# Kernel optimization log

Hardware: AMD Instinct MI355X
Metric: run time of the kernel (lower is better)

The kernel has to match this reference:

```python
import jax, jax.numpy as jnp
import numpy as np

N_WIRES = 14
N_LAYERS = 2
BATCH = 128


def _ry(t):
    # t: scalar or (B,) real angle -> (...,2,2) complex64 RY matrix
    c = jnp.cos(t / 2)
    s = jnp.sin(t / 2)
    m = jnp.stack([jnp.stack([c, -s], -1), jnp.stack([s, c], -1)], -2)
    return m.astype(jnp.complex64)


def _rz(t):
    tc = t.astype(jnp.complex64) if hasattr(t, 'astype') else jnp.asarray(t, jnp.complex64)
    em = jnp.exp(-0.5j * tc)
    ep = jnp.exp(0.5j * tc)
    z = jnp.zeros_like(em)
    return jnp.stack([jnp.stack([em, z], -1), jnp.stack([z, ep], -1)], -2)


def _rx(t):
    c = jnp.cos(t / 2).astype(jnp.complex64)
    s = (-1j) * jnp.sin(t / 2).astype(jnp.complex64)
    return jnp.stack([jnp.stack([c, s], -1), jnp.stack([s, c], -1)], -2)


def _apply_1q(state, mat, w, n):
    # state: (B, 2**n), wire 0 = most significant axis (Pennylane convention)
    B = state.shape[0]
    s = state.reshape(B, 2 ** w, 2, -1)
    if mat.ndim == 2:
        s = jnp.einsum('ij,bajc->baic', mat, s)
    else:  # per-batch matrices (data encoding)
        s = jnp.einsum('bij,bajc->baic', mat, s)
    return s.reshape(B, -1)


def _apply_cnot(state, c, t, n):
    B = state.shape[0]
    p, q = (c, t) if c < t else (t, c)
    s = state.reshape(B, 2 ** p, 2, 2 ** (q - p - 1), 2, 2 ** (n - q - 1))
    if c < t:
        # control at axis 2, target at axis 4; flip target where control==1
        s = jnp.stack([s[:, :, 0], jnp.flip(s[:, :, 1], axis=3)], axis=2)
    else:
        # control at axis 4, target at axis 2
        s = jnp.stack([s[:, :, :, :, 0], jnp.flip(s[:, :, :, :, 1], axis=2)], axis=4)
    return s.reshape(B, -1)


def _circuit(x, params):
    B, n = x.shape
    n_layers = params.shape[0]
    state = jnp.zeros((B, 2 ** n), dtype=jnp.complex64).at[:, 0].set(1.0)
    # data encoding: RY(x[:, w]) on each wire (batched gate matrices)
    for w in range(n):
        state = _apply_1q(state, _ry(x[:, w]), w, n)
    for l in range(n_layers):
        for w in range(n):
            state = _apply_1q(state, _ry(params[l, w, 0]), w, n)
            state = _apply_1q(state, _rz(params[l, w, 1]), w, n)
            state = _apply_1q(state, _rx(params[l, w, 2]), w, n)
        for w in range(n - 1):
            state = _apply_cnot(state, w, w + 1, n)
        state = _apply_cnot(state, n - 1, 0, n)
    probs = state.real ** 2 + state.imag ** 2  # (B, 2**n)
    zs = []
    for w in range(n):
        p = probs.reshape(B, 2 ** w, 2, -1)
        zs.append(p[:, :, 0].sum(axis=(1, 2)) - p[:, :, 1].sum(axis=(1, 2)))
    return jnp.stack(zs, axis=1).astype(jnp.float32)  # (B, n) <Z_w>


def setup_inputs() -> dict:
    key = jax.random.key(0)
    kx, kp = jax.random.split(key)
    x = jax.random.normal(kx, (BATCH, N_WIRES), dtype=jnp.float32)
    params = jax.random.normal(kp, (N_LAYERS, N_WIRES, 3), dtype=jnp.float32)
    return {"x": x, "params": params}


def reference(x, params):
    return _circuit(x, params)
```

## Files before the change

### kernel.cpp

```cpp
#include <hip/hip_runtime.h>

#define NW 14
#define NT 1024
#define BATCH 128

typedef float v2f __attribute__((ext_vector_type(2)));

constexpr unsigned cnot_pc(unsigned j, int c, int t) {
  int pc = 13 - c, pt = 13 - t;
  return j ^ (((j >> pc) & 1u) << pt);
}
constexpr unsigned gperm(unsigned j) {
  j = cnot_pc(j, 13, 0);
  for (int w = 12; w >= 0; --w) j = cnot_pc(j, w, w + 1);
  return j;
}
constexpr unsigned topbit(unsigned x) {
  unsigned h = 1;
  while (x >>= 1) h <<= 1;
  return h;
}

struct CT {
  unsigned M[NW], S[NW], R[NW];
  static constexpr void inv(const unsigned col[NW], unsigned out[NW]) {
    unsigned rm[NW] = {}, ri[NW] = {};
    for (int r = 0; r < NW; ++r) { rm[r] = 0; ri[r] = 1u << r; }
    for (int b = 0; b < NW; ++b)
      for (int r = 0; r < NW; ++r) rm[r] |= ((col[b] >> r) & 1u) << b;
    for (int c = 0; c < NW; ++c) {
      int piv = c;
      while (!((rm[piv] >> c) & 1u)) ++piv;
      unsigned tm = rm[c]; rm[c] = rm[piv]; rm[piv] = tm;
      unsigned ti = ri[c]; ri[c] = ri[piv]; ri[piv] = ti;
      for (int r = 0; r < NW; ++r)
        if (r != c && ((rm[r] >> c) & 1u)) { rm[r] ^= rm[c]; ri[r] ^= ri[c]; }
    }
    for (int r = 0; r < NW; ++r) out[r] = ri[r];
  }
  constexpr CT() : M{}, S{}, R{} {
    unsigned c1[NW] = {}, c2[NW] = {};
    for (int b = 0; b < NW; ++b) { c1[b] = gperm(1u << b); c2[b] = gperm(c1[b]); }
    unsigned i1[NW] = {}, i2[NW] = {};
    inv(c1, i1); inv(c2, i2);
    for (int w = 0; w < NW; ++w) { M[w] = c1[13 - w]; S[w] = i1[13 - w]; R[w] = i2[13 - w]; }
  }
};
static constexpr CT qct{};
static_assert(qct.M[0] == 0x3000u && qct.M[12] == 0x3u && qct.M[13] == 0x3001u, "mask check");
static_assert(qct.M[4] == 0x300u, "mask check");

__device__ __forceinline__ v2f vswap(v2f m) {
  v2f r;
  r.x = -m.y;
  r.y = m.x;
  return r;
}
__device__ __forceinline__ v2f cmulv(v2f a, v2f b) {
  v2f r;
  r.x = fmaf(a.x, b.x, -a.y * b.y);
  r.y = fmaf(a.x, b.y, a.y * b.x);
  return r;
}

__device__ __forceinline__ void make_mat(float ay, float az, float ax_, v2f m[4]) {
  float c, s, ct, st, cr, sr;
  __sincosf(0.5f * ay, &s, &c);
  __sincosf(0.5f * az, &st, &ct);
  __sincosf(0.5f * ax_, &sr, &cr);
  v2f em, ep;
  em.x = ct; em.y = -st;
  ep.x = ct; ep.y = st;
  v2f r00 = c * em, r01 = -s * em, r10 = s * ep, r11 = c * ep;
  v2f isr;
  isr.x = 0.f; isr.y = -sr;
  m[0] = cmulv(isr, r10) + cr * r00;
  m[1] = cmulv(isr, r11) + cr * r01;
  m[2] = cmulv(isr, r00) + cr * r10;
  m[3] = cmulv(isr, r01) + cr * r11;
}

template <int CTRL> __device__ __forceinline__ int dppi(int x) {
  return __builtin_amdgcn_update_dpp(0, x, CTRL, 0xF, 0xF, true);
}
template <unsigned LM> __device__ __forceinline__ float lane_xor1(float x) {
  if constexpr (LM == 0u) return x;
  else if constexpr (LM >= 16u) {
    return __shfl_xor(x, (int)LM, 64);
  } else {
    int v = __float_as_int(x);
    if constexpr ((LM & 0xCu) == 0xCu) v = dppi<0x140>(v);
    else if constexpr ((LM & 0xCu) == 0x4u) v = dppi<0x141>(v);
    else if constexpr ((LM & 0xCu) == 0x8u) v = dppi<0x128>(v);
    constexpr unsigned REM = ((LM & 0xCu) == 0xCu)   ? (LM ^ 0xFu)
                             : ((LM & 0xCu) == 0x4u) ? (LM ^ 0x7u)
                             : ((LM & 0xCu) == 0x8u) ? (LM ^ 0x8u)
                                                     : LM;
    if constexpr (REM != 0u) {
      constexpr int QC = (int)((0u ^ REM) | ((1u ^ REM) << 2) | ((2u ^ REM) << 4) |
                               ((3u ^ REM) << 6));
      v = dppi<QC>(v);
    }
    return __int_as_float(v);
  }
}
template <unsigned LM> __device__ __forceinline__ v2f lane_xor2(v2f v) {
  if constexpr (LM == 0u) return v;
  v2f r;
  r.x = lane_xor1<LM>(v.x);
  r.y = lane_xor1<LM>(v.y);
  return r;
}

template <unsigned RM, unsigned LM, unsigned SR>
__device__ __forceinline__ void gate16(v2f (&a)[16], const v2f* gm, const v2f* gs,
                                       bool st_) {
  const v2f e00 = gm[0], e01 = gm[1], e10 = gm[2], e11 = gm[3];
  const v2f s00 = gs[0], s01 = gs[1], s10 = gs[2], s11 = gs[3];
  const v2f f00 = st_ ? e11 : e00, f01 = st_ ? e10 : e01;
  const v2f f10 = st_ ? e01 : e10, f11 = st_ ? e00 : e11;
  const v2f h00 = st_ ? s11 : s00, h01 = st_ ? s10 : s01;
  const v2f h10 = st_ ? s01 : s10, h11 = st_ ? s00 : s11;
  if constexpr (RM == 0u) {
#pragma unroll
    for (int r = 0; r < 16; ++r) {
      const v2f p = lane_xor2<LM>(a[r]);
      const v2f A = a[r];
      if (__builtin_popcount((unsigned)r & SR) & 1)
        a[r] = A.x * f11 + A.y * h11 + p.x * f10 + p.y * h10;
      else
        a[r] = A.x * f00 + A.y * h00 + p.x * f01 + p.y * h01;
    }
  } else {
    constexpr unsigned HB = topbit(RM);
#pragma unroll
    for (int r = 0; r < 16; ++r) {
      if (r & (int)HB) continue;
      const int r2 = r ^ (int)RM;
      const v2f A = a[r], B = a[r2];
      const v2f pA = lane_xor2<LM>(B), pB = lane_xor2<LM>(A);
      a[r] = (__builtin_popcount((unsigned)r & SR) & 1)
                 ? (A.x * f11 + A.y * h11 + pA.x * f10 + pA.y * h10)
                 : (A.x * f00 + A.y * h00 + pA.x * f01 + pA.y * h01);
      a[r2] = (__builtin_popcount((unsigned)r2 & SR) & 1)
                  ? (B.x * f11 + B.y * h11 + pB.x * f10 + pB.y * h10)
                  : (B.x * f00 + B.y * h00 + pB.x * f01 + pB.y * h01);
    }
  }
}

template <int W>
__device__ __forceinline__ void applyP1(v2f (&a)[16], const v2f* gm, const v2f* gs,
                                        unsigned qb) {
  constexpr unsigned M = qct.M[W], S = qct.S[W];
  static_assert((M & ~0x3FFu) == 0u, "P1 gate out of window");
  gate16<(M & 0xFu), ((M >> 4) & 0x3Fu), (S & 0xFu)>(a, gm, gs, (__popc(qb & S) & 1) != 0);
}
template <int W>
__device__ __forceinline__ void applyP2(v2f (&a)[16], const v2f* gm, const v2f* gs,
                                        unsigned qb) {
  constexpr unsigned M = qct.M[W], S = qct.S[W];
  static_assert((M & ~0x3E01u) == 0u, "P2 gate out of window");
  gate16<((M >> 10) & 0xFu), ((M & 1u) | (((M >> 9) & 1u) << 1)), ((S >> 10) & 0xFu)>(
      a, gm, gs, (__popc(qb & S) & 1) != 0);
}

__global__ __launch_bounds__(NT, 4) void qsim(const float* __restrict__ x,
                                              const float* __restrict__ params,
                                              float* __restrict__ out) {
  __shared__ v2f stx[16384];
  __shared__ v2f v0[NW][2];
  __shared__ v2f g1m[NW][4];
  __shared__ v2f g1s[NW][4];
  __shared__ v2f Ahi[128];
  __shared__ v2f BloP[8][17];
  __shared__ float red[16][NW];

  const int bat = blockIdx.x;
  const int t = threadIdx.x;
  const unsigned ln = (unsigned)t & 63u, wv = (unsigned)t >> 6;

  if (t < 2 * NW) {
    const int layer = (t >= NW);
    const int w = t - layer * NW;
    v2f m[4];
    if (!layer) {
      make_mat(params[w * 3 + 0] + x[bat * NW + w], params[w * 3 + 1], params[w * 3 + 2], m);
      v0[w][0] = m[0];
      v0[w][1] = m[2];
    } else {
      make_mat(params[NW * 3 + w * 3 + 0], params[NW * 3 + w * 3 + 1],
               params[NW * 3 + w * 3 + 2], m);
      g1m[w][0] = m[0]; g1m[w][1] = m[1]; g1m[w][2] = m[2]; g1m[w][3] = m[3];
      g1s[w][0] = vswap(m[0]); g1s[w][1] = vswap(m[1]);
      g1s[w][2] = vswap(m[2]); g1s[w][3] = vswap(m[3]);
    }
  }
  __syncthreads();
  if (t < 128) {
    v2f pa; pa.x = 1.f; pa.y = 0.f;
#pragma unroll
    for (int w = 0; w < 7; ++w) pa = cmulv(pa, v0[w][(t >> (6 - w)) & 1]);
    Ahi[t] = pa;
    v2f pb; pb.x = 1.f; pb.y = 0.f;
#pragma unroll
    for (int w = 7; w < 14; ++w) pb = cmulv(pb, v0[w][(t >> (13 - w)) & 1]);
    BloP[t >> 4][t & 15] = pb;
  }
  __syncthreads();

  v2f a[16];
  {
    const v2f ahi = Ahi[(wv << 3) | (ln >> 3)];
    const v2f ahis = vswap(ahi);
#pragma unroll
    for (int r = 0; r < 16; ++r) {
      const v2f b = BloP[ln & 7][r];
      a[r] = b.x * ahi + b.y * ahis;
    }
  }

  const unsigned qb1 = (ln << 4) | (wv << 10);
  applyP1<12>(a, g1m[12], g1s[12], qb1);
  applyP1<11>(a, g1m[11], g1s[11], qb1);
  applyP1<10>(a, g1m[10], g1s[10], qb1);
  applyP1<9>(a, g1m[9], g1s[9], qb1);
  applyP1<8>(a, g1m[8], g1s[8], qb1);
  applyP1<7>(a, g1m[7], g1s[7], qb1);
  applyP1<6>(a, g1m[6], g1s[6], qb1);
  applyP1<5>(a, g1m[5], g1s[5], qb1);
  applyP1<4>(a, g1m[4], g1s[4], qb1);

  {
    const unsigned bw = (wv << 10) | (ln << 4) | (ln & 0xFu);
#pragma unroll
    for (int r = 0; r < 16; ++r) stx[bw ^ (unsigned)r] = a[r];
  }
  __syncthreads();
  const unsigned qb2 = (ln & 1u) | (((ln >> 2) & 0xFu) << 1) | (wv << 5) |
                       (((ln >> 1) & 1u) << 9);
  {
    const unsigned c2 = ((ln >> 5) & 1u) | ((wv & 7u) << 1);
    const unsigned br = qb2 ^ c2;
#pragma unroll
    for (int r = 0; r < 16; ++r) a[r] = stx[br | ((unsigned)r << 10)];
  }

  applyP2<3>(a, g1m[3], g1s[3], qb2);
  applyP2<2>(a, g1m[2], g1s[2], qb2);
  applyP2<1>(a, g1m[1], g1s[1], qb2);
  applyP2<0>(a, g1m[0], g1s[0], qb2);
  applyP2<13>(a, g1m[13], g1s[13], qb2);

  float T[16];
#pragma unroll
  for (int r = 0; r < 16; ++r) T[r] = fmaf(a[r].x, a[r].x, a[r].y * a[r].y);
#pragma unroll
  for (int s = 1; s < 16; s <<= 1) {
#pragma unroll
    for (int r = 0; r < 16; ++r) {
      if (!(r & s)) {
        float u = T[r], v = T[r ^ s];
        T[r] = u + v;
        T[r ^ s] = u - v;
      }
    }
  }

#pragma unroll
  for (int w = 0; w < NW; ++w) {
    constexpr unsigned Rr[NW] = {qct.R[0], qct.R[1], qct.R[2], qct.R[3], qct.R[4],
                                 qct.R[5], qct.R[6], qct.R[7], qct.R[8], qct.R[9],
                                 qct.R[10], qct.R[11], qct.R[12], qct.R[13]};
    const unsigned R = Rr[w];
    float val = T[(R >> 10) & 0xFu];
    val = (__popc(qb2 & R) & 1) ? -val : val;
    val += lane_xor1<1>(val);
    val += lane_xor1<2>(val);
    { float u = lane_xor1<4>(val); val += u; }
    val += lane_xor1<8>(val);
    val += __shfl_xor(val, 16, 64);
    val += __shfl_xor(val, 32, 64);
    if ((t & 63) == 0) red[wv][w] = val;
  }
  __syncthreads();
  if (t < NW) {
    float s = 0.f;
#pragma unroll
    for (int i = 0; i < 16; ++i) s += red[i][t];
    out[bat * NW + t] = s;
  }
}

extern "C" void kernel_launch(void* const* d_in, const int* in_sizes, int n_in,
                              void* d_out, int out_size, void* d_ws, size_t ws_size,
                              hipStream_t stream) {
  (void)in_sizes; (void)n_in; (void)d_ws; (void)ws_size; (void)out_size;
  const float* x = (const float*)d_in[0];
  const float* params = (const float*)d_in[1];
  float* out = (float*)d_out;
  qsim<<<dim3(BATCH), dim3(NT), 0, stream>>>(x, params, out);
}
```

Baseline: 69.90 us.

## Remap state storage into permuted basis so gates become plain register/DPP pairs

Changes the per-thread index mapping so that each layer-1 gate acts on a single register bit or a single lane bit in a transformed basis, instead of on multi-bit XOR masks with parity-dependent coefficient swaps. Gates split into pure in-register butterflies and DPP lane-exchange gates, and the gate matrices are packed as float4 for wider LDS loads. The initial product-state construction, the LDS transpose addressing and the measurement masks are rewritten for the new basis, with constexpr checks to guard correctness. This aims to cut cross-lane shuffles and per-element selects, at the cost of more complex indexing that is only validated by compile-time asserts.

```diff
diff --git a/kernel.cpp b/kernel.cpp
--- a/kernel.cpp
+++ b/kernel.cpp
@@ -15,10 +15,10 @@
   for (int w = 12; w >= 0; --w) j = cnot_pc(j, w, w + 1);
   return j;
 }
-constexpr unsigned topbit(unsigned x) {
-  unsigned h = 1;
-  while (x >>= 1) h <<= 1;
-  return h;
+constexpr int pcnt(unsigned x) {
+  int c = 0;
+  while (x) { c += (int)(x & 1u); x >>= 1; }
+  return c;
 }
 
 struct CT {
@@ -48,7 +48,52 @@
 };
 static constexpr CT qct{};
 static_assert(qct.M[0] == 0x3000u && qct.M[12] == 0x3u && qct.M[13] == 0x3001u, "mask check");
-static_assert(qct.M[4] == 0x300u, "mask check");
+
+constexpr unsigned p1f(unsigned b) {
+  return ((b ^ (b >> 1)) ^ ((b & 1u) * 0x3000u)) & 0x3FFFu;
+}
+constexpr bool chk_p1_formula() {
+  for (unsigned b = 0; b < 16384u; ++b)
+    if (p1f(b) != gperm(b)) return false;
+  return true;
+}
+static_assert(chk_p1_formula(), "P1 closed form == gperm");
+constexpr bool chk_role() {
+  for (int w = 0; w < NW; ++w) {
+    for (unsigned b = 0; b < 16384u; b += 37u)
+      if ((unsigned)(pcnt(p1f(b) & qct.S[w]) & 1) != ((b >> (13 - w)) & 1u)) return false;
+    for (int j = 0; j < 14; ++j)
+      if ((unsigned)(pcnt(p1f(1u << j) & qct.S[w]) & 1) != (((1u << j) >> (13 - w)) & 1u))
+        return false;
+  }
+  return true;
+}
+static_assert(chk_role(), "b-space role = storage bit");
+struct RBt {
+  unsigned v[NW];
+  constexpr RBt() : v{} {
+    for (int w = 0; w < NW; ++w) {
+      unsigned m = 0;
+      for (int j = 0; j < 14; ++j)
+        if (pcnt(gperm(1u << j) & qct.R[w]) & 1) m |= 1u << j;
+      v[w] = m;
+    }
+  }
+};
+static constexpr RBt rbt{};
+constexpr bool chk_meas() {
+  for (int w = 0; w < NW; ++w)
+    for (unsigned b = 0; b < 16384u; b += 41u)
+      if ((pcnt(p1f(b) & qct.R[w]) & 1) != (pcnt(b & rbt.v[w]) & 1)) return false;
+  return true;
+}
+static_assert(chk_meas(), "b-space measurement masks");
+constexpr bool chk_cr() {
+  for (unsigned r = 0; r < 16u; ++r)
+    if (p1f(r << 1) != ((r << 1) ^ r) || p1f(r << 1) >= 128u) return false;
+  return true;
+}
+static_assert(chk_cr(), "P1(r<<1) == (r<<1)^r and < 128");
 
 __device__ __forceinline__ v2f vswap(v2f m) {
   v2f r;
@@ -112,57 +157,41 @@
   return r;
 }
 
-template <unsigned RM, unsigned LM, unsigned SR>
-__device__ __forceinline__ void gate16(v2f (&a)[16], const v2f* gm, const v2f* gs,
-                                       bool st_) {
-  const v2f e00 = gm[0], e01 = gm[1], e10 = gm[2], e11 = gm[3];
-  const v2f s00 = gs[0], s01 = gs[1], s10 = gs[2], s11 = gs[3];
-  const v2f f00 = st_ ? e11 : e00, f01 = st_ ? e10 : e01;
-  const v2f f10 = st_ ? e01 : e10, f11 = st_ ? e00 : e11;
-  const v2f h00 = st_ ? s11 : s00, h01 = st_ ? s10 : s01;
-  const v2f h10 = st_ ? s01 : s10, h11 = st_ ? s00 : s11;
-  if constexpr (RM == 0u) {
-#pragma unroll
-    for (int r = 0; r < 16; ++r) {
-      const v2f p = lane_xor2<LM>(a[r]);
-      const v2f A = a[r];
-      if (__builtin_popcount((unsigned)r & SR) & 1)
-        a[r] = A.x * f11 + A.y * h11 + p.x * f10 + p.y * h10;
-      else
-        a[r] = A.x * f00 + A.y * h00 + p.x * f01 + p.y * h01;
-    }
-  } else {
-    constexpr unsigned HB = topbit(RM);
-#pragma unroll
-    for (int r = 0; r < 16; ++r) {
-      if (r & (int)HB) continue;
-      const int r2 = r ^ (int)RM;
-      const v2f A = a[r], B = a[r2];
-      const v2f pA = lane_xor2<LM>(B), pB = lane_xor2<LM>(A);
-      a[r] = (__builtin_popcount((unsigned)r & SR) & 1)
-                 ? (A.x * f11 + A.y * h11 + pA.x * f10 + pA.y * h10)
-                 : (A.x * f00 + A.y * h00 + pA.x * f01 + pA.y * h01);
-      a[r2] = (__builtin_popcount((unsigned)r2 & SR) & 1)
-                  ? (B.x * f11 + B.y * h11 + pB.x * f10 + pB.y * h10)
-                  : (B.x * f00 + B.y * h00 + pB.x * f01 + pB.y * h01);
-    }
-  }
-}
-
-template <int W>
-__device__ __forceinline__ void applyP1(v2f (&a)[16], const v2f* gm, const v2f* gs,
-                                        unsigned qb) {
-  constexpr unsigned M = qct.M[W], S = qct.S[W];
-  static_assert((M & ~0x3FFu) == 0u, "P1 gate out of window");
-  gate16<(M & 0xFu), ((M >> 4) & 0x3Fu), (S & 0xFu)>(a, gm, gs, (__popc(qb & S) & 1) != 0);
-}
-template <int W>
-__device__ __forceinline__ void applyP2(v2f (&a)[16], const v2f* gm, const v2f* gs,
-                                        unsigned qb) {
-  constexpr unsigned M = qct.M[W], S = qct.S[W];
-  static_assert((M & ~0x3E01u) == 0u, "P2 gate out of window");
-  gate16<((M >> 10) & 0xFu), ((M & 1u) | (((M >> 9) & 1u) << 1)), ((S >> 10) & 0xFu)>(
-      a, gm, gs, (__popc(qb & S) & 1) != 0);
+
+template <unsigned RM>
+__device__ __forceinline__ void gate_reg(v2f (&a)[16], const float4* G) {
+  const float4 A0 = G[0], A1 = G[1], A2 = G[2], A3 = G[3];
+  v2f m00, m01, m10, m11, s00, s01, s10, s11;
+  m00.x = A0.x; m00.y = A0.y; m01.x = A0.z; m01.y = A0.w;
+  m10.x = A1.x; m10.y = A1.y; m11.x = A1.z; m11.y = A1.w;
+  s00.x = A2.x; s00.y = A2.y; s01.x = A2.z; s01.y = A2.w;
+  s10.x = A3.x; s10.y = A3.y; s11.x = A3.z; s11.y = A3.w;
+#pragma unroll
+  for (int r = 0; r < 16; ++r) {
+    if (r & (int)RM) continue;
+    const int r1 = r | (int)RM;
+    const v2f A = a[r], B = a[r1];
+    a[r] = A.x * m00 + A.y * s00 + B.x * m01 + B.y * s01;
+    a[r1] = A.x * m10 + A.y * s10 + B.x * m11 + B.y * s11;
+  }
+}
+
+template <unsigned LM>
+__device__ __forceinline__ void gate_dpp(v2f (&a)[16], const float4* G, bool role) {
+  const float4 A0 = G[0], A1 = G[1], A2 = G[2], A3 = G[3];
+  v2f m00, m01, m10, m11, s00, s01, s10, s11;
+  m00.x = A0.x; m00.y = A0.y; m01.x = A0.z; m01.y = A0.w;
+  m10.x = A1.x; m10.y = A1.y; m11.x = A1.z; m11.y = A1.w;
+  s00.x = A2.x; s00.y = A2.y; s01.x = A2.z; s01.y = A2.w;
+  s10.x = A3.x; s10.y = A3.y; s11.x = A3.z; s11.y = A3.w;
+  const v2f f0 = role ? m11 : m00, f0s = role ? s11 : s00;
+  const v2f f1 = role ? m10 : m01, f1s = role ? s10 : s01;
+#pragma unroll
+  for (int r = 0; r < 16; ++r) {
+    const v2f P = lane_xor2<LM>(a[r]);
+    const v2f A = a[r];
+    a[r] = A.x * f0 + A.y * f0s + P.x * f1 + P.y * f1s;
+  }
 }
 
 __global__ __launch_bounds__(NT, 4) void qsim(const float* __restrict__ x,
@@ -170,8 +199,7 @@
                                               float* __restrict__ out) {
   __shared__ v2f stx[16384];
   __shared__ v2f v0[NW][2];
-  __shared__ v2f g1m[NW][4];
-  __shared__ v2f g1s[NW][4];
+  __shared__ float4 gq[NW][4];
   __shared__ v2f Ahi[128];
   __shared__ v2f BloP[8][17];
   __shared__ float red[16][NW];
@@ -191,9 +219,11 @@
     } else {
       make_mat(params[NW * 3 + w * 3 + 0], params[NW * 3 + w * 3 + 1],
                params[NW * 3 + w * 3 + 2], m);
-      g1m[w][0] = m[0]; g1m[w][1] = m[1]; g1m[w][2] = m[2]; g1m[w][3] = m[3];
-      g1s[w][0] = vswap(m[0]); g1s[w][1] = vswap(m[1]);
-      g1s[w][2] = vswap(m[2]); g1s[w][3] = vswap(m[3]);
+      const v2f s0 = vswap(m[0]), s1 = vswap(m[1]), s2 = vswap(m[2]), s3 = vswap(m[3]);
+      gq[w][0] = make_float4(m[0].x, m[0].y, m[1].x, m[1].y);
+      gq[w][1] = make_float4(m[2].x, m[2].y, m[3].x, m[3].y);
+      gq[w][2] = make_float4(s0.x, s0.y, s1.x, s1.y);
+      gq[w][3] = make_float4(s2.x, s2.y, s3.x, s3.y);
     }
   }
   __syncthreads();
@@ -209,48 +239,52 @@
   }
   __syncthreads();
 
+  const unsigned bb = (ln << 5) | ((wv & 7u) << 11) | (wv >> 3);
+  const unsigned qb = ((bb ^ (bb >> 1)) ^ ((bb & 1u) * 0x3000u)) & 0x3FFFu;
+
   v2f a[16];
   {
-    const v2f ahi = Ahi[(wv << 3) | (ln >> 3)];
+    const v2f ahi = Ahi[qb >> 7];
     const v2f ahis = vswap(ahi);
+    const unsigned q7 = qb & 127u;
 #pragma unroll
     for (int r = 0; r < 16; ++r) {
-      const v2f b = BloP[ln & 7][r];
+      const unsigned j = q7 ^ (((unsigned)r << 1) ^ (unsigned)r);
+      const v2f b = BloP[j >> 4][j & 15u];
       a[r] = b.x * ahi + b.y * ahis;
     }
   }
 
-  const unsigned qb1 = (ln << 4) | (wv << 10);
-  applyP1<12>(a, g1m[12], g1s[12], qb1);
-  applyP1<11>(a, g1m[11], g1s[11], qb1);
-  applyP1<10>(a, g1m[10], g1s[10], qb1);
-  applyP1<9>(a, g1m[9], g1s[9], qb1);
-  applyP1<8>(a, g1m[8], g1s[8], qb1);
-  applyP1<7>(a, g1m[7], g1s[7], qb1);
-  applyP1<6>(a, g1m[6], g1s[6], qb1);
-  applyP1<5>(a, g1m[5], g1s[5], qb1);
-  applyP1<4>(a, g1m[4], g1s[4], qb1);
+  gate_reg<1>(a, gq[12]);
+  gate_reg<2>(a, gq[11]);
+  gate_reg<4>(a, gq[10]);
+  gate_reg<8>(a, gq[9]);
+  gate_dpp<1>(a, gq[8], (ln & 1u) != 0);
+  gate_dpp<2>(a, gq[7], (ln & 2u) != 0);
+  gate_dpp<4>(a, gq[6], (ln & 4u) != 0);
+  gate_dpp<8>(a, gq[5], (ln & 8u) != 0);
 
   {
-    const unsigned bw = (wv << 10) | (ln << 4) | (ln & 0xFu);
-#pragma unroll
-    for (int r = 0; r < 16; ++r) stx[bw ^ (unsigned)r] = a[r];
+    const unsigned bw = bb ^ ((ln & 0xFu) << 1);
+#pragma unroll
+    for (int r = 0; r < 16; ++r) stx[bw ^ ((unsigned)r << 1)] = a[r];
   }
   __syncthreads();
-  const unsigned qb2 = (ln & 1u) | (((ln >> 2) & 0xFu) << 1) | (wv << 5) |
-                       (((ln >> 1) & 1u) << 9);
+  const unsigned brb = (wv << 1) | (((ln >> 2) & 0xFu) << 5) | ((ln & 1u) << 9) |
+                       (((ln >> 1) & 1u) << 10);
   {
-    const unsigned c2 = ((ln >> 5) & 1u) | ((wv & 7u) << 1);
-    const unsigned br = qb2 ^ c2;
-#pragma unroll
-    for (int r = 0; r < 16; ++r) a[r] = stx[br | ((unsigned)r << 10)];
-  }
-
-  applyP2<3>(a, g1m[3], g1s[3], qb2);
-  applyP2<2>(a, g1m[2], g1s[2], qb2);
-  applyP2<1>(a, g1m[1], g1s[1], qb2);
-  applyP2<0>(a, g1m[0], g1s[0], qb2);
-  applyP2<13>(a, g1m[13], g1s[13], qb2);
+    const unsigned br = brb ^ (((brb >> 5) & 0xFu) << 1);
+#pragma unroll
+    for (int r = 0; r < 16; ++r)
+      a[r] = stx[br | (((unsigned)r & 7u) << 11) | ((unsigned)r >> 3)];
+  }
+
+  gate_dpp<1>(a, gq[4], (ln & 1u) != 0);
+  gate_dpp<2>(a, gq[3], (ln & 2u) != 0);
+  gate_reg<1>(a, gq[2]);
+  gate_reg<2>(a, gq[1]);
+  gate_reg<4>(a, gq[0]);
+  gate_reg<8>(a, gq[13]);
 
   float T[16];
 #pragma unroll
@@ -269,12 +303,14 @@
 
 #pragma unroll
   for (int w = 0; w < NW; ++w) {
-    constexpr unsigned Rr[NW] = {qct.R[0], qct.R[1], qct.R[2], qct.R[3], qct.R[4],
-                                 qct.R[5], qct.R[6], qct.R[7], qct.R[8], qct.R[9],
-                                 qct.R[10], qct.R[11], qct.R[12], qct.R[13]};
+    constexpr unsigned Rr[NW] = {rbt.v[0], rbt.v[1], rbt.v[2], rbt.v[3], rbt.v[4],
+                                 rbt.v[5], rbt.v[6], rbt.v[7], rbt.v[8], rbt.v[9],
+                                 rbt.v[10], rbt.v[11], rbt.v[12], rbt.v[13]};
     const unsigned R = Rr[w];
-    float val = T[(R >> 10) & 0xFu];
-    val = (__popc(qb2 & R) & 1) ? -val : val;
+    const unsigned m = ((R >> 11) & 1u) | (((R >> 12) & 1u) << 1) | (((R >> 13) & 1u) << 2) |
+                       ((R & 1u) << 3);
+    float val = T[m];
+    val = (__popc(brb & R) & 1) ? -val : val;
     val += lane_xor1<1>(val);
     val += lane_xor1<2>(val);
     { float u = lane_xor1<4>(val); val += u; }
```

Measured after the change: 68.29 us. -2.3%, faster.
